# Performance work log

Measured on AMD Instinct MI355X. Metric: run time of the kernel, lower is better.

Reference implementation:

```python
import jax, jax.numpy as jnp
import numpy as np

B, L, C, K, F = 32, 8192, 128, 7, 128


def setup_inputs() -> dict:
    key = jax.random.key(0)
    kx, kw = jax.random.split(key)
    x = jax.random.normal(kx, (B, L, C, 1), dtype=jnp.float32)
    # glorot-style scale for the learned kernel [K, C, F]
    scale = jnp.sqrt(2.0 / (K * C + F)).astype(jnp.float32)
    kernel = jax.random.normal(kw, (K, C, F), dtype=jnp.float32) * scale
    return {"x": x, "kernel": kernel}


def reference(x, kernel):
    # x: [B, L, C, 1]; kernel: [K, C, F]
    # Original loop computes out[b,i,f] = sum_{k,c} x[b,i+k,c,0] * kernel[k,c,f]
    # which is a valid-padding 1D convolution.
    xs = x[..., 0]  # [B, L, C]
    out = jax.lax.conv_general_dilated(
        xs, kernel,
        window_strides=(1,),
        padding="VALID",
        dimension_numbers=("NWC", "WIO", "NWC"),
    )  # [B, L-K+1, F]
    return out[..., None]  # [B, L-K+1, F, 1]
```

## Files before the change

### kernel.cpp

```cpp
#include <hip/hip_runtime.h>
#include <hip/hip_bf16.h>

#define BATCH 32
#define LEN   8192
#define CDIM  128
#define TAPS  7
#define FDIM  128
#define LOUT  (LEN - TAPS + 1)
#define BM    128
#define XROWS (BM + TAPS - 1)
#define NCHUNK (TAPS * 2)

typedef __attribute__((ext_vector_type(8)))  short bf16x8;
typedef __attribute__((ext_vector_type(16))) float f32x16;

static __device__ __forceinline__ unsigned short bf16_rne(float f) {
    unsigned u = __float_as_uint(f);
    u += 0x7FFFu + ((u >> 16) & 1u);
    return (unsigned short)(u >> 16);
}
static __device__ __forceinline__ unsigned pack2(float a, float b) {
    return (unsigned)bf16_rne(a) | ((unsigned)bf16_rne(b) << 16);
}

__global__ void wconv_kernel(const float* __restrict__ w, ushort* __restrict__ wt) {
    int idx = blockIdx.x * 256 + threadIdx.x;
    int k = idx >> 14;
    int rem = idx & 16383;
    int f = rem >> 7;
    int c = rem & 127;
    wt[idx] = bf16_rne(w[(k << 14) + (c << 7) + f]);
}

__global__ __launch_bounds__(256, 2)
void conv_gemm_kernel(const float* __restrict__ x, const ushort* __restrict__ wt,
                      float* __restrict__ out) {
    __shared__ __align__(16) ushort Xs[XROWS * CDIM];
    __shared__ __align__(16) ushort Ws[2][FDIM * 64];

    const int tid  = threadIdx.x;
    const int lane = tid & 63;
    const int wid  = tid >> 6;
    const int wm   = wid >> 1;
    const int wn   = wid & 1;
    const int l31  = lane & 31;
    const int l5   = lane >> 5;

    const int bid  = blockIdx.x;
    const int b    = bid >> 6;
    const int i0   = (bid & 63) * BM;

    const float* xb = x + (size_t)b * LEN * CDIM;

    auto stage_w = [&](int idx) {
        const ushort* wsrc = wt + (idx >> 1) * (FDIM * CDIM) + (idx & 1) * 64;
        ushort* wbuf = Ws[idx & 1];
        #pragma unroll
        for (int it = 0; it < 4; ++it) {
            int s  = it * 256 + tid;
            int f  = s >> 3;
            int jp = s & 7;
            int j  = jp ^ (f & 7);
            const ushort* g = wsrc + f * CDIM + j * 8;
            ushort* l = &wbuf[(it * 256 + (tid & 192)) * 8];
            __builtin_amdgcn_global_load_lds(
                (const __attribute__((address_space(1))) void*)g,
                (__attribute__((address_space(3))) void*)l, 16, 0, 0);
        }
    };

    stage_w(0);

    #pragma unroll
    for (int it = 0; it < 9; ++it) {
        int q = it * 256 + tid;
        if (q < XROWS * 16) {
            int r   = q >> 4;
            int col = q & 15;
            int gi  = i0 + r;
            float4 v0, v1;
            if (gi < LEN) {
                const float4* p = (const float4*)(xb + (size_t)gi * CDIM + col * 8);
                v0 = p[0]; v1 = p[1];
            } else {
                v0 = make_float4(0.f, 0.f, 0.f, 0.f);
                v1 = v0;
            }
            int scol = col ^ (r & 15);
            uint4 pk;
            pk.x = pack2(v0.x, v0.y);
            pk.y = pack2(v0.z, v0.w);
            pk.z = pack2(v1.x, v1.y);
            pk.w = pack2(v1.z, v1.w);
            *(uint4*)&Xs[r * CDIM + scol * 8] = pk;
        }
    }

    f32x16 acc[2][2] = {};

    const int f0 = (wn << 6) + l31;
    const int f1 = f0 + 32;
    const int swz0 = f0 & 7;
    const int swz1 = f1 & 7;

    #pragma unroll
    for (int idx = 0; idx < NCHUNK; ++idx) {
        __syncthreads();
        if (idx + 1 < NCHUNK) stage_w(idx + 1);

        const int t = idx >> 1;
        const int h = idx & 1;
        const ushort* wb = Ws[idx & 1];
        const int r0 = (wm << 6) + l31 + t;
        const int r1 = r0 + 32;

        #pragma unroll
        for (int kk = 0; kk < 4; ++kk) {
            int jl = kk * 2 + l5;
            int jg = h * 8 + jl;
            bf16x8 a0 = *(const bf16x8*)&Xs[r0 * CDIM + ((jg ^ (r0 & 15)) << 3)];
            bf16x8 a1 = *(const bf16x8*)&Xs[r1 * CDIM + ((jg ^ (r1 & 15)) << 3)];
            bf16x8 b0 = *(const bf16x8*)&wb[f0 * 64 + ((jl ^ swz0) << 3)];
            bf16x8 b1 = *(const bf16x8*)&wb[f1 * 64 + ((jl ^ swz1) << 3)];
            acc[0][0] = __builtin_amdgcn_mfma_f32_32x32x16_bf16(a0, b0, acc[0][0], 0, 0, 0);
            acc[0][1] = __builtin_amdgcn_mfma_f32_32x32x16_bf16(a0, b1, acc[0][1], 0, 0, 0);
            acc[1][0] = __builtin_amdgcn_mfma_f32_32x32x16_bf16(a1, b0, acc[1][0], 0, 0, 0);
            acc[1][1] = __builtin_amdgcn_mfma_f32_32x32x16_bf16(a1, b1, acc[1][1], 0, 0, 0);
        }
    }

    float* ob = out + (size_t)b * LOUT * FDIM;
    #pragma unroll
    for (int fm = 0; fm < 2; ++fm) {
        #pragma unroll
        for (int fn = 0; fn < 2; ++fn) {
            #pragma unroll
            for (int r = 0; r < 16; ++r) {
                int row = (wm << 6) + (fm << 5) + (r & 3) + ((r >> 2) << 3) + (l5 << 2);
                int i = i0 + row;
                if (i < LOUT) {
                    ob[(size_t)i * FDIM + (wn << 6) + (fn << 5) + l31] = acc[fm][fn][r];
                }
            }
        }
    }
}

extern "C" void kernel_launch(void* const* d_in, const int* in_sizes, int n_in,
                              void* d_out, int out_size, void* d_ws, size_t ws_size,
                              hipStream_t stream) {
    const float* x = (const float*)d_in[0];
    const float* w = (const float*)d_in[1];
    float* out = (float*)d_out;
    ushort* wt = (ushort*)d_ws;

    wconv_kernel<<<448, 256, 0, stream>>>(w, wt);
    conv_gemm_kernel<<<BATCH * 64, 256, 0, stream>>>(x, wt, out);
}
```

Baseline: 272.4 us.

## Triple-buffer weight staging with 512-thread blocks and 256-row tiles

The output tile grows from 128 to 256 rows, served by 512-thread blocks with eight waves, which halves the block count and shrinks the relative halo overhead of the input rows. Weight chunks are now prefetched two steps ahead into a three-slot LDS ring. Explicit vmcnt/lgkmcnt waits replace the per-chunk __syncthreads, so global-to-LDS loads overlap more of the MFMA work. The MFMA section runs under raised wave priority via s_setprio. The larger LDS footprint and block size may lower occupancy, and the hand-written waitcnt counts must match the number of outstanding loads to stay correct.

```diff
diff --git a/kernel.cpp b/kernel.cpp
--- a/kernel.cpp
+++ b/kernel.cpp
@@ -7,9 +7,10 @@
 #define TAPS  7
 #define FDIM  128
 #define LOUT  (LEN - TAPS + 1)
-#define BM    128
+#define BM    256
 #define XROWS (BM + TAPS - 1)
 #define NCHUNK (TAPS * 2)
+#define NBUF  3
 
 typedef __attribute__((ext_vector_type(8)))  short bf16x8;
 typedef __attribute__((ext_vector_type(16))) float f32x16;
@@ -32,11 +33,11 @@
     wt[idx] = bf16_rne(w[(k << 14) + (c << 7) + f]);
 }
 
-__global__ __launch_bounds__(256, 2)
+__global__ __launch_bounds__(512, 2)
 void conv_gemm_kernel(const float* __restrict__ x, const ushort* __restrict__ wt,
                       float* __restrict__ out) {
     __shared__ __align__(16) ushort Xs[XROWS * CDIM];
-    __shared__ __align__(16) ushort Ws[2][FDIM * 64];
+    __shared__ __align__(16) ushort Ws[NBUF][FDIM * 64];
 
     const int tid  = threadIdx.x;
     const int lane = tid & 63;
@@ -47,33 +48,32 @@
     const int l5   = lane >> 5;
 
     const int bid  = blockIdx.x;
-    const int b    = bid >> 6;
-    const int i0   = (bid & 63) * BM;
+    const int b    = bid >> 5;
+    const int i0   = (bid & 31) * BM;
 
     const float* xb = x + (size_t)b * LEN * CDIM;
 
-    auto stage_w = [&](int idx) {
+    auto stage_w = [&](int idx, ushort* wbuf) {
         const ushort* wsrc = wt + (idx >> 1) * (FDIM * CDIM) + (idx & 1) * 64;
-        ushort* wbuf = Ws[idx & 1];
         #pragma unroll
-        for (int it = 0; it < 4; ++it) {
-            int s  = it * 256 + tid;
+        for (int it = 0; it < 2; ++it) {
+            int s  = it * 512 + tid;
             int f  = s >> 3;
             int jp = s & 7;
             int j  = jp ^ (f & 7);
             const ushort* g = wsrc + f * CDIM + j * 8;
-            ushort* l = &wbuf[(it * 256 + (tid & 192)) * 8];
+            ushort* l = &wbuf[(it * 512 + (tid & 448)) * 8];
             __builtin_amdgcn_global_load_lds(
                 (const __attribute__((address_space(1))) void*)g,
                 (__attribute__((address_space(3))) void*)l, 16, 0, 0);
         }
     };
 
-    stage_w(0);
+    stage_w(0, Ws[0]);
 
     #pragma unroll
     for (int it = 0; it < 9; ++it) {
-        int q = it * 256 + tid;
+        int q = it * 512 + tid;
         if (q < XROWS * 16) {
             int r   = q >> 4;
             int col = q & 15;
@@ -96,36 +96,49 @@
         }
     }
 
+    stage_w(1, Ws[1]);
+
+    asm volatile("s_waitcnt vmcnt(2) lgkmcnt(0)" ::: "memory");
+    __builtin_amdgcn_s_barrier();
+
     f32x16 acc[2][2] = {};
 
     const int f0 = (wn << 6) + l31;
     const int f1 = f0 + 32;
-    const int swz0 = f0 & 7;
-    const int swz1 = f1 & 7;
+    const int swz = l31 & 7;
 
     #pragma unroll
     for (int idx = 0; idx < NCHUNK; ++idx) {
-        __syncthreads();
-        if (idx + 1 < NCHUNK) stage_w(idx + 1);
+        if (idx + 2 < NCHUNK) stage_w(idx + 2, Ws[(idx + 2) % NBUF]);
 
         const int t = idx >> 1;
         const int h = idx & 1;
-        const ushort* wb = Ws[idx & 1];
+        const ushort* wb = Ws[idx % NBUF];
         const int r0 = (wm << 6) + l31 + t;
         const int r1 = r0 + 32;
 
+        __builtin_amdgcn_s_setprio(1);
         #pragma unroll
         for (int kk = 0; kk < 4; ++kk) {
             int jl = kk * 2 + l5;
             int jg = h * 8 + jl;
             bf16x8 a0 = *(const bf16x8*)&Xs[r0 * CDIM + ((jg ^ (r0 & 15)) << 3)];
             bf16x8 a1 = *(const bf16x8*)&Xs[r1 * CDIM + ((jg ^ (r1 & 15)) << 3)];
-            bf16x8 b0 = *(const bf16x8*)&wb[f0 * 64 + ((jl ^ swz0) << 3)];
-            bf16x8 b1 = *(const bf16x8*)&wb[f1 * 64 + ((jl ^ swz1) << 3)];
+            bf16x8 b0 = *(const bf16x8*)&wb[f0 * 64 + ((jl ^ swz) << 3)];
+            bf16x8 b1 = *(const bf16x8*)&wb[f1 * 64 + ((jl ^ swz) << 3)];
             acc[0][0] = __builtin_amdgcn_mfma_f32_32x32x16_bf16(a0, b0, acc[0][0], 0, 0, 0);
             acc[0][1] = __builtin_amdgcn_mfma_f32_32x32x16_bf16(a0, b1, acc[0][1], 0, 0, 0);
             acc[1][0] = __builtin_amdgcn_mfma_f32_32x32x16_bf16(a1, b0, acc[1][0], 0, 0, 0);
             acc[1][1] = __builtin_amdgcn_mfma_f32_32x32x16_bf16(a1, b1, acc[1][1], 0, 0, 0);
+        }
+        __builtin_amdgcn_s_setprio(0);
+
+        if (idx + 2 < NCHUNK) {
+            asm volatile("s_waitcnt vmcnt(2) lgkmcnt(0)" ::: "memory");
+            __builtin_amdgcn_s_barrier();
+        } else if (idx + 1 < NCHUNK) {
+            asm volatile("s_waitcnt vmcnt(0) lgkmcnt(0)" ::: "memory");
+            __builtin_amdgcn_s_barrier();
         }
     }
 
@@ -155,5 +168,5 @@
     ushort* wt = (ushort*)d_ws;
 
     wconv_kernel<<<448, 256, 0, stream>>>(w, wt);
-    conv_gemm_kernel<<<BATCH * 64, 256, 0, stream>>>(x, wt, out);
+    conv_gemm_kernel<<<BATCH * 32, 512, 0, stream>>>(x, wt, out);
 }
```

Result: no change. 273.6 us (+0.4%).

## Load weights directly from global in MFMA fragment layout, drop LDS staging

Applied to the files above, without the earlier changes.

The weight-conversion kernel now writes bf16 weights pre-permuted into the exact per-lane MFMA B-fragment order. The GEMM kernel reads B operands straight from global memory (L2-resident) instead of double-buffering them through LDS, which removes the per-chunk __syncthreads barriers and frees LDS. Launch bounds are raised to four blocks per SM to increase occupancy. The trade-off is that every B fragment now costs a global load on the inner-loop critical path, relying on L2 hits and latency hiding through higher occupancy.

```diff
diff --git a/kernel.cpp b/kernel.cpp
--- a/kernel.cpp
+++ b/kernel.cpp
@@ -24,19 +24,21 @@
 }
 
 __global__ void wconv_kernel(const float* __restrict__ w, ushort* __restrict__ wt) {
-    int idx = blockIdx.x * 256 + threadIdx.x;
-    int k = idx >> 14;
-    int rem = idx & 16383;
-    int f = rem >> 7;
-    int c = rem & 127;
-    wt[idx] = bf16_rne(w[(k << 14) + (c << 7) + f]);
+    int i = blockIdx.x * 256 + threadIdx.x;
+    int e  = i & 7;
+    int f  = (i >> 3) & 127;
+    int l5 = (i >> 10) & 1;
+    int kk = (i >> 11) & 3;
+    int h  = (i >> 13) & 1;
+    int t  = i >> 14;
+    int c  = h * 64 + kk * 16 + l5 * 8 + e;
+    wt[i] = bf16_rne(w[(t << 14) + (c << 7) + f]);
 }
 
-__global__ __launch_bounds__(256, 2)
+__global__ __launch_bounds__(256, 4)
 void conv_gemm_kernel(const float* __restrict__ x, const ushort* __restrict__ wt,
                       float* __restrict__ out) {
     __shared__ __align__(16) ushort Xs[XROWS * CDIM];
-    __shared__ __align__(16) ushort Ws[2][FDIM * 64];
 
     const int tid  = threadIdx.x;
     const int lane = tid & 63;
@@ -51,25 +53,6 @@
     const int i0   = (bid & 63) * BM;
 
     const float* xb = x + (size_t)b * LEN * CDIM;
-
-    auto stage_w = [&](int idx) {
-        const ushort* wsrc = wt + (idx >> 1) * (FDIM * CDIM) + (idx & 1) * 64;
-        ushort* wbuf = Ws[idx & 1];
-        #pragma unroll
-        for (int it = 0; it < 4; ++it) {
-            int s  = it * 256 + tid;
-            int f  = s >> 3;
-            int jp = s & 7;
-            int j  = jp ^ (f & 7);
-            const ushort* g = wsrc + f * CDIM + j * 8;
-            ushort* l = &wbuf[(it * 256 + (tid & 192)) * 8];
-            __builtin_amdgcn_global_load_lds(
-                (const __attribute__((address_space(1))) void*)g,
-                (__attribute__((address_space(3))) void*)l, 16, 0, 0);
-        }
-    };
-
-    stage_w(0);
 
     #pragma unroll
     for (int it = 0; it < 9; ++it) {
@@ -95,24 +78,21 @@
             *(uint4*)&Xs[r * CDIM + scol * 8] = pk;
         }
     }
+    __syncthreads();
 
     f32x16 acc[2][2] = {};
 
     const int f0 = (wn << 6) + l31;
-    const int f1 = f0 + 32;
-    const int swz0 = f0 & 7;
-    const int swz1 = f1 & 7;
+
+    const ushort* wp = wt + (l5 << 10) + (f0 << 3);
 
     #pragma unroll
     for (int idx = 0; idx < NCHUNK; ++idx) {
-        __syncthreads();
-        if (idx + 1 < NCHUNK) stage_w(idx + 1);
-
         const int t = idx >> 1;
         const int h = idx & 1;
-        const ushort* wb = Ws[idx & 1];
         const int r0 = (wm << 6) + l31 + t;
         const int r1 = r0 + 32;
+        const ushort* wpi = wp + idx * 8192;
 
         #pragma unroll
         for (int kk = 0; kk < 4; ++kk) {
@@ -120,8 +100,8 @@
             int jg = h * 8 + jl;
             bf16x8 a0 = *(const bf16x8*)&Xs[r0 * CDIM + ((jg ^ (r0 & 15)) << 3)];
             bf16x8 a1 = *(const bf16x8*)&Xs[r1 * CDIM + ((jg ^ (r1 & 15)) << 3)];
-            bf16x8 b0 = *(const bf16x8*)&wb[f0 * 64 + ((jl ^ swz0) << 3)];
-            bf16x8 b1 = *(const bf16x8*)&wb[f1 * 64 + ((jl ^ swz1) << 3)];
+            bf16x8 b0 = *(const bf16x8*)&wpi[kk * 2048];
+            bf16x8 b1 = *(const bf16x8*)&wpi[kk * 2048 + 256];
             acc[0][0] = __builtin_amdgcn_mfma_f32_32x32x16_bf16(a0, b0, acc[0][0], 0, 0, 0);
             acc[0][1] = __builtin_amdgcn_mfma_f32_32x32x16_bf16(a0, b1, acc[0][1], 0, 0, 0);
             acc[1][0] = __builtin_amdgcn_mfma_f32_32x32x16_bf16(a1, b0, acc[1][0], 0, 0, 0);
```

Result: faster. 265.1 us (-2.7%).
